# Kernel tuning notes

Measured on AMD Instinct MI355X. Metric: run time of the kernel, lower is better.

The kernel has to match this reference:

```python
import jax, jax.numpy as jnp
import numpy as np

D_MODEL = 1024
NUM_HEADS = 16
D_K = D_MODEL // NUM_HEADS


def setup_inputs() -> dict:
    key = jax.random.key(0)
    ks = jax.random.split(key, 11)
    B, S = 2, 2048
    s = 1.0 / np.sqrt(D_MODEL)
    return {
        "q": jax.random.normal(ks[0], (B, S, D_MODEL), jnp.float32),
        "k": jax.random.normal(ks[1], (B, S, D_MODEL), jnp.float32),
        "v": jax.random.normal(ks[2], (B, S, D_MODEL), jnp.float32),
        "w_q": jax.random.normal(ks[3], (D_MODEL, D_MODEL), jnp.float32) * s,
        "b_q": jnp.zeros((D_MODEL,), jnp.float32),
        "w_k": jax.random.normal(ks[4], (D_MODEL, D_MODEL), jnp.float32) * s,
        "b_k": jnp.zeros((D_MODEL,), jnp.float32),
        "w_v": jax.random.normal(ks[5], (D_MODEL, D_MODEL), jnp.float32) * s,
        "b_v": jnp.zeros((D_MODEL,), jnp.float32),
        "w_o": jax.random.normal(ks[6], (D_MODEL, D_MODEL), jnp.float32) * s,
        "b_o": jnp.zeros((D_MODEL,), jnp.float32),
    }


def reference(q, k, v, w_q, b_q, w_k, b_k, w_v, b_v, w_o, b_o):
    B, S, _ = q.shape
    H, Dk = NUM_HEADS, D_K

    def split_heads(x):  # [B,S,D] -> [B,H,S,Dk]
        return x.reshape(B, S, H, Dk).transpose(0, 2, 1, 3)

    # torch nn.Linear: x @ W.T + b
    qh = split_heads(q @ w_q.T + b_q)
    kh = split_heads(k @ w_k.T + b_k)
    vh = split_heads(v @ w_v.T + b_v)

    scale = 1.0 / jnp.sqrt(jnp.asarray(Dk, qh.dtype))
    scores = jnp.einsum("bhsd,bhtd->bhst", qh, kh) * scale  # [B,H,S,S]
    attn = jax.nn.softmax(scores, axis=-1)
    # dropout is identity in eval/deterministic baseline
    out = jnp.einsum("bhst,bhtd->bhsd", attn, vh)  # [B,H,S,Dk]
    out = out.transpose(0, 2, 1, 3).reshape(B, S, H * Dk)
    return out @ w_o.T + b_o
```

## Files before the change

kernel.cpp:

```cpp
#include <hip/hip_runtime.h>
#include <hip/hip_bf16.h>
#include <stdint.h>

typedef unsigned short u16;
typedef __attribute__((ext_vector_type(8))) short short8;
typedef __attribute__((ext_vector_type(8))) __bf16 bf16x8;
typedef __attribute__((ext_vector_type(4))) float f32x4;
typedef __attribute__((ext_vector_type(4))) uint32_t u32x4;

#if defined(__has_builtin)
#if __has_builtin(__builtin_amdgcn_global_load_lds)
#define USE_GLLDS 1
#endif
#endif

#if defined(__has_builtin)
#if __has_builtin(__builtin_amdgcn_exp2f)
#define HAVE_EXP2_BUILTIN 1
#endif
#endif
__device__ __forceinline__ float fexp2(float x) {
#ifdef HAVE_EXP2_BUILTIN
  return __builtin_amdgcn_exp2f(x);
#else
  return exp2f(x);
#endif
}

__device__ __forceinline__ u16 f2bf(float f) {
  __hip_bfloat16 h = __float2bfloat16(f);
  return __builtin_bit_cast(u16, h);
}

__device__ __forceinline__ f32x4 mfma16(bf16x8 a, bf16x8 b, f32x4 c) {
  return __builtin_amdgcn_mfma_f32_16x16x32_bf16(a, b, c, 0, 0, 0);
}

#ifdef USE_GLLDS
__device__ __forceinline__ void async_cp16(const void* g, void* l) {
  __builtin_amdgcn_global_load_lds(
      (const __attribute__((address_space(1))) void*)g,
      (__attribute__((address_space(3))) void*)l, 16, 0, 0);
}
#endif

__global__ __launch_bounds__(256) void cvt_all(
    const float* __restrict__ q, const float* __restrict__ k,
    const float* __restrict__ v, const float* __restrict__ w0,
    const float* __restrict__ w1, const float* __restrict__ w2,
    const float* __restrict__ w3, u16* __restrict__ dst) {
  size_t i = ((size_t)blockIdx.x * 256 + threadIdx.x) * 8;
  const size_t M1 = 1u << 20;
  const float* s;
  size_t base;
  if (i < 4 * M1) { s = q; base = 0; }
  else if (i < 8 * M1) { s = k; base = 4 * M1; }
  else if (i < 12 * M1) { s = v; base = 8 * M1; }
  else if (i < 13 * M1) { s = w0; base = 12 * M1; }
  else if (i < 14 * M1) { s = w1; base = 13 * M1; }
  else if (i < 15 * M1) { s = w2; base = 14 * M1; }
  else { s = w3; base = 15 * M1; }
  const float4 a = *(const float4*)(s + (i - base));
  const float4 b = *(const float4*)(s + (i - base) + 4);
  short8 r;
  r[0] = (short)f2bf(a.x); r[1] = (short)f2bf(a.y);
  r[2] = (short)f2bf(a.z); r[3] = (short)f2bf(a.w);
  r[4] = (short)f2bf(b.x); r[5] = (short)f2bf(b.y);
  r[6] = (short)f2bf(b.z); r[7] = (short)f2bf(b.w);
  *(short8*)(dst + i) = r;
}

__device__ __forceinline__ void gemm_body(const u16* __restrict__ X,
                                          const u16* __restrict__ W,
                                          const float* __restrict__ bias,
                                          void* __restrict__ outp, int mode) {
  __shared__ u16 Al[128 * 64];
  __shared__ u16 Bl[128 * 64];
  const int tid = threadIdx.x;
  const int wv = tid >> 6, l = tid & 63;
  const int wr = wv >> 1, wc = wv & 1;
  const int m0 = blockIdx.y * 128, n0 = blockIdx.x * 128;
  const int lrow = l & 15, lk = (l >> 4) * 8;

  f32x4 acc[4][4];
#pragma unroll
  for (int i = 0; i < 4; ++i)
#pragma unroll
    for (int j = 0; j < 4; ++j) acc[i][j] = (f32x4){0.f, 0.f, 0.f, 0.f};

  const u16* Asrc = X + (size_t)(m0 + (tid >> 3)) * 1024 + (tid & 7) * 8;
  const u16* Bsrc = W + (size_t)(n0 + (tid >> 3)) * 1024 + (tid & 7) * 8;

  for (int kt = 0; kt < 1024; kt += 64) {
#ifdef USE_GLLDS
#pragma unroll
    for (int p = 0; p < 4; ++p) {
      async_cp16(Asrc + (size_t)p * 32 * 1024 + kt, &Al[p * 2048 + wv * 512]);
      async_cp16(Bsrc + (size_t)p * 32 * 1024 + kt, &Bl[p * 2048 + wv * 512]);
    }
#else
    short8 ar[4], br[4];
#pragma unroll
    for (int p = 0; p < 4; ++p) {
      ar[p] = *(const short8*)(Asrc + (size_t)p * 32 * 1024 + kt);
      br[p] = *(const short8*)(Bsrc + (size_t)p * 32 * 1024 + kt);
    }
#pragma unroll
    for (int p = 0; p < 4; ++p) {
      *(short8*)&Al[p * 2048 + tid * 8] = ar[p];
      *(short8*)&Bl[p * 2048 + tid * 8] = br[p];
    }
#endif
    __syncthreads();
#pragma unroll
    for (int ks = 0; ks < 2; ++ks) {
      bf16x8 af[4], bf[4];
#pragma unroll
      for (int mf = 0; mf < 4; ++mf)
        af[mf] = *(const bf16x8*)&Al[(wr * 64 + mf * 16 + lrow) * 64 + ks * 32 + lk];
#pragma unroll
      for (int nf = 0; nf < 4; ++nf)
        bf[nf] = *(const bf16x8*)&Bl[(wc * 64 + nf * 16 + lrow) * 64 + ks * 32 + lk];
#pragma unroll
      for (int mf = 0; mf < 4; ++mf)
#pragma unroll
        for (int nf = 0; nf < 4; ++nf)
          acc[mf][nf] = mfma16(af[mf], bf[nf], acc[mf][nf]);
    }
    __syncthreads();
  }

  const int rb = (l >> 4) * 4;
#pragma unroll
  for (int mf = 0; mf < 4; ++mf) {
#pragma unroll
    for (int nf = 0; nf < 4; ++nf) {
      const int gn = n0 + wc * 64 + nf * 16 + lrow;
      const float bi = bias[gn];
#pragma unroll
      for (int r = 0; r < 4; ++r) {
        const int gm = m0 + wr * 64 + mf * 16 + rb + r;
        float val = acc[mf][nf][r] + bi;
        const int b = gm >> 11, s = gm & 2047, h = gn >> 6, d = gn & 63;
        if (mode == 3) {
          ((float*)outp)[(size_t)gm * 1024 + gn] = val;
        } else if (mode == 2) {
          ((u16*)outp)[(((size_t)((b * 16 + h) * 64 + d)) << 11) + s] = f2bf(val);
        } else {
          if (mode == 0) val *= 0.18033688f;
          ((u16*)outp)[(((size_t)((b * 16 + h) * 2048 + s)) << 6) + d] = f2bf(val);
        }
      }
    }
  }
}

__global__ __launch_bounds__(256) void gemm_proj(
    const u16* __restrict__ qb, const u16* __restrict__ wqb,
    const float* __restrict__ b_q, const float* __restrict__ b_k,
    const float* __restrict__ b_v, u16* __restrict__ Qh) {
  const int z = blockIdx.z;
  const float* bias = (z == 0) ? b_q : ((z == 1) ? b_k : b_v);
  gemm_body(qb + ((size_t)z << 22), wqb + ((size_t)z << 20), bias,
            Qh + ((size_t)z << 22), z);
}

__global__ __launch_bounds__(256) void gemm_out(
    const u16* __restrict__ X, const u16* __restrict__ W,
    const float* __restrict__ bias, float* __restrict__ out) {
  gemm_body(X, W, bias, out, 3);
}

__global__ __launch_bounds__(512, 4) void flash_attn3(
    const u16* __restrict__ Qh, const u16* __restrict__ Kh,
    const u16* __restrict__ VT, u16* __restrict__ Op,
    float2* __restrict__ ml) {
  __shared__ __align__(16) u16 Kbuf[4096];
  __shared__ __align__(16) u16 Vbuf[4096];
  __shared__ __align__(16) uint32_t Pl[8 * 576];

  const int tid = threadIdx.x;
  const int wv = tid >> 6, l = tid & 63;
  const int q = l & 15, g = l >> 4;
  const int qt = blockIdx.x, bh = blockIdx.y, z = blockIdx.z;

  const u16* Qp = Qh + ((size_t)bh * 2048 + qt * 128 + wv * 16) * 64;
  const u16* Kp = Kh + (size_t)bh * 2048 * 64;
  const u16* Vp = VT + (size_t)bh * 64 * 2048;

  bf16x8 qf[2];
  qf[0] = *(const bf16x8*)(Qp + q * 64 + g * 8);
  qf[1] = *(const bf16x8*)(Qp + q * 64 + 32 + g * 8);

  f32x4 o[4];
#pragma unroll
  for (int df = 0; df < 4; ++df) o[df] = (f32x4){0.f, 0.f, 0.f, 0.f};
  float m = -1e30f, ls = 0.f;

  const int srow = l >> 3;
  const int scolq = (l & 7) ^ srow;
  const int pbase = wv * 576 + q * 36;
  const char* kb = (const char*)&Kbuf[0];
  const char* vb = (const char*)&Vbuf[0];
  const int rsw = (q & 7) << 4;

#ifdef USE_GLLDS
#define STAGE(t)                                                              \
  do {                                                                        \
    const int n0_ = (t) * 64;                                                 \
    const u16* kg_ = Kp + (size_t)(n0_ + wv * 8 + srow) * 64 + scolq * 8;     \
    const u16* vg_ = Vp + (size_t)(wv * 8 + srow) * 2048 + n0_ + scolq * 8;   \
    async_cp16(kg_, &Kbuf[wv * 512]);                                         \
    async_cp16(vg_, &Vbuf[wv * 512]);                                         \
  } while (0)
#else
#define STAGE(t)                                                              \
  do {                                                                        \
    const int n0_ = (t) * 64;                                                 \
    const u16* kg_ = Kp + (size_t)(n0_ + wv * 8 + srow) * 64 + scolq * 8;     \
    const u16* vg_ = Vp + (size_t)(wv * 8 + srow) * 2048 + n0_ + scolq * 8;   \
    short8 kt_ = *(const short8*)kg_;                                         \
    short8 vt_ = *(const short8*)vg_;                                         \
    *(short8*)&Kbuf[wv * 512 + l * 8] = kt_;                                  \
    *(short8*)&Vbuf[wv * 512 + l * 8] = vt_;                                  \
  } while (0)
#endif

  const int t0 = z * 16;
  for (int tt = 0; tt < 16; ++tt) {
    STAGE(t0 + tt);
    __syncthreads();

    f32x4 s[4];
#pragma unroll
    for (int nj = 0; nj < 4; ++nj) s[nj] = (f32x4){0.f, 0.f, 0.f, 0.f};
#pragma unroll
    for (int ks = 0; ks < 2; ++ks) {
#pragma unroll
      for (int nj = 0; nj < 4; ++nj) {
        bf16x8 kf = *(const bf16x8*)(kb + (nj * 16 + q) * 128 +
                                     (((ks * 4 + g) << 4) ^ rsw));
        s[nj] = mfma16(kf, qf[ks], s[nj]);
      }
    }

    const float a0 = fmaxf(fmaxf(s[0][0], s[0][1]), fmaxf(s[0][2], s[0][3]));
    const float a1 = fmaxf(fmaxf(s[1][0], s[1][1]), fmaxf(s[1][2], s[1][3]));
    const float a2 = fmaxf(fmaxf(s[2][0], s[2][1]), fmaxf(s[2][2], s[2][3]));
    const float a3 = fmaxf(fmaxf(s[3][0], s[3][1]), fmaxf(s[3][2], s[3][3]));
    float mt = fmaxf(fmaxf(a0, a1), fmaxf(a2, a3));
    mt = fmaxf(mt, __shfl_xor(mt, 16));
    mt = fmaxf(mt, __shfl_xor(mt, 32));
    if (!__all(mt <= m + 8.f)) {
      const float nm = fmaxf(m, mt);
      const float rf = fexp2(m - nm);
      m = nm;
      ls *= rf;
#pragma unroll
      for (int df = 0; df < 4; ++df) o[df] *= rf;
    }
    float ps = 0.f;
#pragma unroll
    for (int nj = 0; nj < 4; ++nj)
#pragma unroll
      for (int r = 0; r < 4; ++r) {
        s[nj][r] = fexp2(s[nj][r] - m);
        ps += s[nj][r];
      }
    ps += __shfl_xor(ps, 16);
    ps += __shfl_xor(ps, 32);
    ls += ps;

#pragma unroll
    for (int nj = 0; nj < 4; ++nj)
#pragma unroll
      for (int pp = 0; pp < 2; ++pp) {
        uint32_t w = (uint32_t)f2bf(s[nj][2 * pp]) |
                     ((uint32_t)f2bf(s[nj][2 * pp + 1]) << 16);
        Pl[pbase + nj * 8 + g * 2 + pp] = w;
      }

#pragma unroll
    for (int ks = 0; ks < 2; ++ks) {
      u32x4 pw = *(const u32x4*)&Pl[pbase + ks * 16 + 4 * g];
      bf16x8 pf = __builtin_bit_cast(bf16x8, pw);
#pragma unroll
      for (int df = 0; df < 4; ++df) {
        bf16x8 vf = *(const bf16x8*)(vb + (df * 16 + q) * 128 +
                                     (((ks * 4 + g) << 4) ^ rsw));
        o[df] = mfma16(vf, pf, o[df]);
      }
    }
    __syncthreads();
  }

  const float inv = 1.f / ls;
  const int rowb = qt * 128 + wv * 16 + q;
  const size_t prow = (size_t)(z * 32 + bh) * 2048 + rowb;
  u16* Po = Op + (prow << 6);
#pragma unroll
  for (int df = 0; df < 4; ++df)
#pragma unroll
    for (int pp = 0; pp < 2; ++pp) {
      uint32_t w = (uint32_t)f2bf(o[df][2 * pp] * inv) |
                   ((uint32_t)f2bf(o[df][2 * pp + 1] * inv) << 16);
      *(uint32_t*)(Po + df * 16 + 4 * g + 2 * pp) = w;
    }
  if (g == 0) ml[prow] = make_float2(m, ls);
}

__global__ __launch_bounds__(256) void combine(
    const uint32_t* __restrict__ Op32, const float2* __restrict__ ml,
    u16* __restrict__ AO) {
  const int j = blockIdx.x * 256 + threadIdx.x;
  const int rowid = j >> 5, w5 = j & 31;
  const float2 a = ml[rowid];
  const float2 c = ml[(1 << 16) + rowid];
  const float M = fmaxf(a.x, c.x);
  float w1 = a.y * fexp2(a.x - M);
  float w2 = c.y * fexp2(c.x - M);
  const float inv = 1.f / (w1 + w2);
  w1 *= inv;
  w2 *= inv;
  const uint32_t p1 = Op32[j];
  const uint32_t p2 = Op32[(1u << 21) + j];
  const float lo = w1 * __builtin_bit_cast(float, p1 << 16) +
                   w2 * __builtin_bit_cast(float, p2 << 16);
  const float hi = w1 * __builtin_bit_cast(float, p1 & 0xffff0000u) +
                   w2 * __builtin_bit_cast(float, p2 & 0xffff0000u);
  const uint32_t outw = (uint32_t)f2bf(lo) | ((uint32_t)f2bf(hi) << 16);
  const int bh = rowid >> 11, s = rowid & 2047, b = bh >> 4, h = bh & 15;
  ((uint32_t*)AO)[((size_t)(b * 2048 + s) << 9) + h * 32 + w5] = outw;
}

extern "C" void kernel_launch(void* const* d_in, const int* in_sizes, int n_in,
                              void* d_out, int out_size, void* d_ws,
                              size_t ws_size, hipStream_t stream) {
  const float* q = (const float*)d_in[0];
  const float* k = (const float*)d_in[1];
  const float* v = (const float*)d_in[2];
  const float* w_q = (const float*)d_in[3];
  const float* b_q = (const float*)d_in[4];
  const float* w_k = (const float*)d_in[5];
  const float* b_k = (const float*)d_in[6];
  const float* w_v = (const float*)d_in[7];
  const float* b_v = (const float*)d_in[8];
  const float* w_o = (const float*)d_in[9];
  const float* b_o = (const float*)d_in[10];

  u16* ws = (u16*)d_ws;
  u16* qb = ws;
  u16* wqb = ws + (12u << 20);
  u16* wob = ws + (15u << 20);
  u16* Qh = ws + (16u << 20);
  u16* Kh = ws + (20u << 20);
  u16* VT = ws + (24u << 20);
  u16* AO = ws + (28u << 20);
  u16* Op = ws;
  float2* ml = (float2*)(ws + (8u << 20));

  cvt_all<<<dim3(8192), dim3(256), 0, stream>>>(q, k, v, w_q, w_k, w_v, w_o, ws);
  gemm_proj<<<dim3(8, 32, 3), dim3(256), 0, stream>>>(qb, wqb, b_q, b_k, b_v, Qh);
  flash_attn3<<<dim3(16, 32, 2), dim3(512), 0, stream>>>(Qh, Kh, VT, Op, ml);
  combine<<<dim3(8192), dim3(256), 0, stream>>>((const uint32_t*)Op, ml, AO);
  gemm_out<<<dim3(8, 32), dim3(256), 0, stream>>>(AO, wob, b_o, (float*)d_out);
}
```

Measured before the change: 173.9 us.

## Register-prefetch next K/V tile in flash attention and remap block order

```diff
diff --git a/kernel.cpp b/kernel.cpp
--- a/kernel.cpp
+++ b/kernel.cpp
@@ -171,7 +171,7 @@
   gemm_body(X, W, bias, out, 3);
 }
 
-__global__ __launch_bounds__(512, 4) void flash_attn3(
+__global__ __launch_bounds__(512, 4) void flash_attn4(
     const u16* __restrict__ Qh, const u16* __restrict__ Kh,
     const u16* __restrict__ VT, u16* __restrict__ Op,
     float2* __restrict__ ml) {
@@ -182,7 +182,10 @@
   const int tid = threadIdx.x;
   const int wv = tid >> 6, l = tid & 63;
   const int q = l & 15, g = l >> 4;
-  const int qt = blockIdx.x, bh = blockIdx.y, z = blockIdx.z;
+
+  const int s_lin = blockIdx.x + (blockIdx.y << 4) + (blockIdx.z << 9);
+  const int o = ((s_lin & 7) << 7) + (s_lin >> 3);
+  const int qt = o & 15, bh = (o >> 4) & 31, z = o >> 9;
 
   const u16* Qp = Qh + ((size_t)bh * 2048 + qt * 128 + wv * 16) * 64;
   const u16* Kp = Kh + (size_t)bh * 2048 * 64;
@@ -192,9 +195,9 @@
   qf[0] = *(const bf16x8*)(Qp + q * 64 + g * 8);
   qf[1] = *(const bf16x8*)(Qp + q * 64 + 32 + g * 8);
 
-  f32x4 o[4];
-#pragma unroll
-  for (int df = 0; df < 4; ++df) o[df] = (f32x4){0.f, 0.f, 0.f, 0.f};
+  f32x4 o_acc[4];
+#pragma unroll
+  for (int df = 0; df < 4; ++df) o_acc[df] = (f32x4){0.f, 0.f, 0.f, 0.f};
   float m = -1e30f, ls = 0.f;
 
   const int srow = l >> 3;
@@ -204,32 +207,27 @@
   const char* vb = (const char*)&Vbuf[0];
   const int rsw = (q & 7) << 4;
 
-#ifdef USE_GLLDS
-#define STAGE(t)                                                              \
-  do {                                                                        \
-    const int n0_ = (t) * 64;                                                 \
-    const u16* kg_ = Kp + (size_t)(n0_ + wv * 8 + srow) * 64 + scolq * 8;     \
-    const u16* vg_ = Vp + (size_t)(wv * 8 + srow) * 2048 + n0_ + scolq * 8;   \
-    async_cp16(kg_, &Kbuf[wv * 512]);                                         \
-    async_cp16(vg_, &Vbuf[wv * 512]);                                         \
-  } while (0)
-#else
-#define STAGE(t)                                                              \
-  do {                                                                        \
-    const int n0_ = (t) * 64;                                                 \
-    const u16* kg_ = Kp + (size_t)(n0_ + wv * 8 + srow) * 64 + scolq * 8;     \
-    const u16* vg_ = Vp + (size_t)(wv * 8 + srow) * 2048 + n0_ + scolq * 8;   \
-    short8 kt_ = *(const short8*)kg_;                                         \
-    short8 vt_ = *(const short8*)vg_;                                         \
-    *(short8*)&Kbuf[wv * 512 + l * 8] = kt_;                                  \
-    *(short8*)&Vbuf[wv * 512 + l * 8] = vt_;                                  \
-  } while (0)
-#endif
-
-  const int t0 = z * 16;
+  const u16* kg = Kp + (size_t)(z * 1024 + wv * 8 + srow) * 64 + scolq * 8;
+  const u16* vg = Vp + (size_t)(wv * 8 + srow) * 2048 + z * 1024 + scolq * 8;
+
+  {
+    short8 k0 = *(const short8*)kg;
+    short8 v0 = *(const short8*)vg;
+    *(short8*)&Kbuf[wv * 512 + l * 8] = k0;
+    *(short8*)&Vbuf[wv * 512 + l * 8] = v0;
+  }
+  kg += 64 * 64;
+  vg += 64;
+  __syncthreads();
+
   for (int tt = 0; tt < 16; ++tt) {
-    STAGE(t0 + tt);
-    __syncthreads();
+    short8 kr, vr;
+    if (tt < 15) {
+      kr = *(const short8*)kg;
+      vr = *(const short8*)vg;
+      kg += 64 * 64;
+      vg += 64;
+    }
 
     f32x4 s[4];
 #pragma unroll
@@ -257,7 +255,7 @@
       m = nm;
       ls *= rf;
 #pragma unroll
-      for (int df = 0; df < 4; ++df) o[df] *= rf;
+      for (int df = 0; df < 4; ++df) o_acc[df] *= rf;
     }
     float ps = 0.f;
 #pragma unroll
@@ -288,8 +286,14 @@
       for (int df = 0; df < 4; ++df) {
         bf16x8 vf = *(const bf16x8*)(vb + (df * 16 + q) * 128 +
                                      (((ks * 4 + g) << 4) ^ rsw));
-        o[df] = mfma16(vf, pf, o[df]);
-      }
+        o_acc[df] = mfma16(vf, pf, o_acc[df]);
+      }
+    }
+
+    __syncthreads();
+    if (tt < 15) {
+      *(short8*)&Kbuf[wv * 512 + l * 8] = kr;
+      *(short8*)&Vbuf[wv * 512 + l * 8] = vr;
     }
     __syncthreads();
   }
@@ -302,8 +306,8 @@
   for (int df = 0; df < 4; ++df)
 #pragma unroll
     for (int pp = 0; pp < 2; ++pp) {
-      uint32_t w = (uint32_t)f2bf(o[df][2 * pp] * inv) |
-                   ((uint32_t)f2bf(o[df][2 * pp + 1] * inv) << 16);
+      uint32_t w = (uint32_t)f2bf(o_acc[df][2 * pp] * inv) |
+                   ((uint32_t)f2bf(o_acc[df][2 * pp + 1] * inv) << 16);
       *(uint32_t*)(Po + df * 16 + 4 * g + 2 * pp) = w;
     }
   if (g == 0) ml[prow] = make_float2(m, ls);
@@ -361,7 +365,7 @@
 
   cvt_all<<<dim3(8192), dim3(256), 0, stream>>>(q, k, v, w_q, w_k, w_v, w_o, ws);
   gemm_proj<<<dim3(8, 32, 3), dim3(256), 0, stream>>>(qb, wqb, b_q, b_k, b_v, Qh);
-  flash_attn3<<<dim3(16, 32, 2), dim3(512), 0, stream>>>(Qh, Kh, VT, Op, ml);
+  flash_attn4<<<dim3(16, 32, 2), dim3(512), 0, stream>>>(Qh, Kh, VT, Op, ml);
   combine<<<dim3(8192), dim3(256), 0, stream>>>((const uint32_t*)Op, ml, AO);
   gemm_out<<<dim3(8, 32), dim3(256), 0, stream>>>(AO, wob, b_o, (float*)d_out);
 }
```

Result: no change. 172.2 us (-1.0%).
